# Optimization experiments

Hardware: AMD Instinct MI355X
Metric: run time of the kernel (lower is better)

The kernel has to match this reference:

```python
import jax, jax.numpy as jnp
import numpy as np

HEAD_DIM = 64
NUM_Q_HEADS = 16
NUM_KV_HEADS = 4
MIN_TS = 1.0
MAX_TS = 10000.0


def _timescale(d):
    frac = 2.0 * jnp.arange(d // 2, dtype=jnp.float32) / d
    return MIN_TS * (MAX_TS / MIN_TS) ** frac  # [d/2]


def _rope(v, pos):
    # v: [B,S,H,D] float, pos: [B,S] int
    ts = _timescale(v.shape[-1])
    sinu = pos[:, :, None, None].astype(jnp.float32) / ts  # [B,S,1,D/2]
    sin, cos = jnp.sin(sinu), jnp.cos(sinu)
    x1, x2 = jnp.split(v.astype(jnp.float32), 2, axis=-1)
    return jnp.concatenate([x1 * cos - x2 * sin, x2 * cos + x1 * sin], axis=-1)


def setup_inputs() -> dict:
    key = jax.random.key(0)
    ks = jax.random.split(key, 5)
    B, S, E = 2, 2048, 1024
    Hq, Hk, D = NUM_Q_HEADS, NUM_KV_HEADS, HEAD_DIM
    sc = 0.02
    x = jax.random.normal(ks[0], (B, S, E), dtype=jnp.float32)
    q_pos = jnp.broadcast_to(jnp.arange(S, dtype=jnp.int32), (B, S))
    Wq = jax.random.normal(ks[1], (E, Hq * D), dtype=jnp.float32) * sc
    Wk = jax.random.normal(ks[2], (E, Hk * D), dtype=jnp.float32) * sc
    Wv = jax.random.normal(ks[3], (E, Hk * D), dtype=jnp.float32) * sc
    Wo = jax.random.normal(ks[4], (Hq * D, E), dtype=jnp.float32) * sc
    return {"x": x, "q_pos": q_pos, "Wq": Wq, "Wk": Wk, "Wv": Wv, "Wo": Wo}


def reference(x, q_pos, Wq, Wk, Wv, Wo):
    B, S, E = x.shape
    Hq, Hk, D = NUM_Q_HEADS, NUM_KV_HEADS, HEAD_DIM
    G = Hq // Hk  # gqa groups

    q = (x @ Wq).reshape(B, S, Hq, D)
    k = (x @ Wk).reshape(B, S, Hk, D)
    v = (x @ Wv).reshape(B, S, Hk, D)

    q = _rope(q, q_pos)  # kv_pos defaults to q_pos
    k = _rope(k, q_pos)

    # [B,Hk,G,S,D] grouped query heads vs shared kv heads
    qg = q.transpose(0, 2, 1, 3).reshape(B, Hk, G, S, D)
    kt = k.transpose(0, 2, 1, 3)  # [B,Hk,S,D]
    vt = v.transpose(0, 2, 1, 3)

    # NOTE: original uses scale=1.0 (no 1/sqrt(D))
    scores = jnp.einsum('bhgqd,bhkd->bhgqk', qg, kt)
    probs = jax.nn.softmax(scores, axis=-1)
    out = jnp.einsum('bhgqk,bhkd->bhgqd', probs, vt)  # [B,Hk,G,S,D]
    out = out.reshape(B, Hq, S, D).transpose(0, 2, 1, 3).reshape(B, S, Hq * D)
    return out @ Wo
```

## Files before the change

### kernel.cpp

```cpp
#include <hip/hip_runtime.h>
#include <hip/hip_fp16.h>
#include <math.h>

typedef __attribute__((ext_vector_type(8))) _Float16 half8;
typedef __attribute__((ext_vector_type(4))) _Float16 half4;
typedef __attribute__((ext_vector_type(4))) float f32x4;
typedef __attribute__((ext_vector_type(16))) float f32x16;
typedef __attribute__((ext_vector_type(4))) unsigned uint4v;

#define HQ 16
#define HK 4
#define DH 64
#define NB 2
#define SEQ 2048
#define EDIM 1024
#define KD 1024

__global__ __launch_bounds__(256) void cvt_x_kernel(const float* __restrict__ x,
                                                    _Float16* __restrict__ xh, int n4) {
  int i = blockIdx.x * 256 + threadIdx.x;
  if (i >= n4) return;
  float4 v = ((const float4*)x)[i];
  half4 h;
  h[0] = (_Float16)v.x; h[1] = (_Float16)v.y; h[2] = (_Float16)v.z; h[3] = (_Float16)v.w;
  *(half4*)(xh + (size_t)i * 4) = h;
}

__global__ __launch_bounds__(256) void rope_tab_kernel(const int* __restrict__ qpos,
                                                       float2* __restrict__ tab) {
  int i = blockIdx.x * 256 + threadIdx.x;
  int row = i >> 5, d = i & 31;
  float ang = (float)qpos[row] * expf((float)d * -0.2878231366242558f);
  float sn, cs;
  sincosf(ang, &sn, &cs);
  tab[i] = make_float2(sn, cs);
}

__global__ __launch_bounds__(256) void transpose_w_kernel(const float* __restrict__ W,
                                                          _Float16* __restrict__ WT,
                                                          int N, int row_off) {
  __shared__ float t[64][65];
  int n0 = blockIdx.x * 64, k0 = blockIdx.y * 64;
  int tid = threadIdx.x;
#pragma unroll
  for (int p = 0; p < 4; ++p) {
    int idx = tid + p * 256;
    int r = idx >> 4;
    int c4 = idx & 15;
    float4 v = *(const float4*)(W + (size_t)(k0 + r) * N + n0 + c4 * 4);
    t[r][c4 * 4 + 0] = v.x; t[r][c4 * 4 + 1] = v.y;
    t[r][c4 * 4 + 2] = v.z; t[r][c4 * 4 + 3] = v.w;
  }
  __syncthreads();
#pragma unroll
  for (int p = 0; p < 4; ++p) {
    int idx = tid + p * 256;
    int n = idx >> 4;
    int k4 = idx & 15;
    half4 h;
    h[0] = (_Float16)t[k4 * 4 + 0][n]; h[1] = (_Float16)t[k4 * 4 + 1][n];
    h[2] = (_Float16)t[k4 * 4 + 2][n]; h[3] = (_Float16)t[k4 * 4 + 3][n];
    *(half4*)(WT + (size_t)(row_off + n0 + n) * KD + k0 + k4 * 4) = h;
  }
}

__global__ __launch_bounds__(256) void transpose_v_kernel(const _Float16* __restrict__ vhp,
                                                          _Float16* __restrict__ vtp) {
  __shared__ _Float16 t[64][72];
  int bh = blockIdx.y;
  int s0 = blockIdx.x * 64;
  const _Float16* src = vhp + ((size_t)bh * SEQ + s0) * DH;
  _Float16* dst = vtp + (size_t)bh * DH * SEQ + s0;
  int tid = threadIdx.x;
#pragma unroll
  for (int p = 0; p < 2; ++p) {
    int idx = tid + p * 256;
    int r = idx >> 3, c8 = idx & 7;
    half8 v = *(const half8*)(src + (size_t)r * DH + c8 * 8);
#pragma unroll
    for (int i = 0; i < 8; ++i) t[r][c8 * 8 + i] = v[i];
  }
  __syncthreads();
#pragma unroll
  for (int p = 0; p < 2; ++p) {
    int idx = tid + p * 256;
    int d = idx >> 3, c8 = idx & 7;
    half8 v;
#pragma unroll
    for (int i = 0; i < 8; ++i) v[i] = t[c8 * 8 + i][d];
    *(half8*)(dst + (size_t)d * SEQ + c8 * 8) = v;
  }
}

#define SWZ(r, kb) ((kb) ^ (((r) & 7) << 4))

__global__ __launch_bounds__(256) void gemm_qkv_rope(
    const _Float16* __restrict__ xh, const _Float16* __restrict__ WT,
    const float2* __restrict__ rtab,
    _Float16* __restrict__ qh, _Float16* __restrict__ kh, _Float16* __restrict__ vh) {
  __shared__ char As[128 * 64 * 2];
  __shared__ char Bs[128 * 64 * 2];
  int tid = threadIdx.x, lane = tid & 63, wid = tid >> 6;
  int wr = wid >> 1, wc = wid & 1;
  int bm = blockIdx.x, bn = blockIdx.y;

  const _Float16* Ag = xh + (size_t)bm * 128 * KD;
  const _Float16* Bg = WT + (size_t)bn * 128 * KD;

  f32x4 acc[4][4] = {};

  for (int kt = 0; kt < KD / 64; ++kt) {
#pragma unroll
    for (int p = 0; p < 4; ++p) {
      int idx = tid + p * 256;
      int r = idx >> 3, k8 = idx & 7;
      half8 va = *(const half8*)(Ag + (size_t)r * KD + kt * 64 + k8 * 8);
      *(half8*)(As + r * 128 + SWZ(r, k8 * 16)) = va;
      half8 vb = *(const half8*)(Bg + (size_t)r * KD + kt * 64 + k8 * 8);
      *(half8*)(Bs + r * 128 + SWZ(r, k8 * 16)) = vb;
    }
    __syncthreads();
#pragma unroll
    for (int kk = 0; kk < 2; ++kk) {
      int kb = kk * 64 + (lane >> 4) * 16;
      half8 af[4], bf[4];
#pragma unroll
      for (int mf = 0; mf < 4; ++mf) {
        int r = wr * 64 + mf * 16 + (lane & 15);
        af[mf] = *(const half8*)(As + r * 128 + SWZ(r, kb));
      }
#pragma unroll
      for (int nf = 0; nf < 4; ++nf) {
        int r = wc * 64 + nf * 16 + (lane & 15);
        bf[nf] = *(const half8*)(Bs + r * 128 + SWZ(r, kb));
      }
#pragma unroll
      for (int mf = 0; mf < 4; ++mf)
#pragma unroll
        for (int nf = 0; nf < 4; ++nf)
          acc[mf][nf] = __builtin_amdgcn_mfma_f32_16x16x32_f16(af[mf], bf[nf], acc[mf][nf], 0, 0, 0);
    }
    __syncthreads();
  }

  int col0 = bn * 128 + wc * 64;
  int row_base = bm * 128 + wr * 64;
#pragma unroll
  for (int mf = 0; mf < 4; ++mf) {
#pragma unroll
    for (int j = 0; j < 4; ++j) {
      int row = row_base + mf * 16 + (lane >> 4) * 4 + j;
      int b = row >> 11, s = row & (SEQ - 1);
      if (col0 < 1024) {
        int hq = col0 >> 6;
        size_t base = (((size_t)b * HQ + hq) * SEQ + s) * DH;
#pragma unroll
        for (int nf = 0; nf < 2; ++nf) {
          int d = nf * 16 + (lane & 15);
          float2 scv = rtab[row * 32 + d];
          float x1 = acc[mf][nf][j], x2 = acc[mf][nf + 2][j];
          qh[base + d]      = (_Float16)(x1 * scv.y - x2 * scv.x);
          qh[base + d + 32] = (_Float16)(x2 * scv.y + x1 * scv.x);
        }
      } else if (col0 < 1280) {
        int hk = (col0 - 1024) >> 6;
        size_t base = (((size_t)b * HK + hk) * SEQ + s) * DH;
#pragma unroll
        for (int nf = 0; nf < 2; ++nf) {
          int d = nf * 16 + (lane & 15);
          float2 scv = rtab[row * 32 + d];
          float x1 = acc[mf][nf][j], x2 = acc[mf][nf + 2][j];
          kh[base + d]      = (_Float16)(x1 * scv.y - x2 * scv.x);
          kh[base + d + 32] = (_Float16)(x2 * scv.y + x1 * scv.x);
        }
      } else {
        int hk = (col0 - 1280) >> 6;
        size_t base = (((size_t)b * HK + hk) * SEQ + s) * DH;
#pragma unroll
        for (int nf = 0; nf < 4; ++nf) {
          int d = nf * 16 + (lane & 15);
          vh[base + d] = (_Float16)acc[mf][nf][j];
        }
      }
    }
  }
}

__global__ __launch_bounds__(256) void attn_kernel(
    const _Float16* __restrict__ qh, const _Float16* __restrict__ kh,
    const _Float16* __restrict__ vt, _Float16* __restrict__ oh) {
  __shared__ char Ks[128 * 64 * 2];
  __shared__ char Vs[64 * 128 * 2];

  int tid = threadIdx.x, lane = tid & 63, wid = tid >> 6;
  int half = lane >> 5, l31 = lane & 31;
  bool lopart = (half == 0);
  int qt = blockIdx.x, bh = blockIdx.y;
  int b = bh >> 4, hq = bh & 15, hk = hq >> 2;

  const _Float16* Qg = qh + (((size_t)b * HQ + hq) * SEQ + qt * 128 + wid * 32 + l31) * DH;
  const _Float16* Kg = kh + (((size_t)b * HK + hk) * SEQ) * DH;
  const _Float16* Vtg = vt + (size_t)(b * HK + hk) * DH * SEQ;

  int kr = tid >> 3, kd8 = tid & 7;
  int vr = tid >> 4, vc8 = tid & 15;

  const _Float16 l2e = (_Float16)1.44269504f;
  half8 qf[4];
#pragma unroll
  for (int ks = 0; ks < 4; ++ks) {
    half8 q0 = *(const half8*)(Qg + ks * 16 + half * 8);
#pragma unroll
    for (int i = 0; i < 8; ++i) q0[i] = q0[i] * l2e;
    qf[ks] = q0;
  }

  f32x16 oacc[2] = {};
  float m = -3e38f, l = 0.f;

  for (int kt = 0; kt < SEQ / 128; ++kt) {
#pragma unroll
    for (int p = 0; p < 4; ++p) {
      int r = kr + p * 32;
      *(half8*)(Ks + r * 128 + SWZ(r, kd8 * 16)) =
          *(const half8*)(Kg + (size_t)(kt * 128 + r) * DH + kd8 * 8);
      int d = vr + p * 16;
      *(half8*)(Vs + d * 256 + SWZ(d, vc8 * 16)) =
          *(const half8*)(Vtg + (size_t)d * SEQ + kt * 128 + vc8 * 8);
    }
    __syncthreads();

    f32x16 sacc[4] = {};
    __builtin_amdgcn_s_setprio(1);
#pragma unroll
    for (int b4 = 0; b4 < 4; ++b4) {
      int r = b4 * 32 + l31;
#pragma unroll
      for (int ks = 0; ks < 4; ++ks) {
        half8 kf = *(const half8*)(Ks + r * 128 + SWZ(r, ks * 32 + half * 16));
        sacc[b4] = __builtin_amdgcn_mfma_f32_32x32x16_f16(kf, qf[ks], sacc[b4], 0, 0, 0);
      }
    }
    __builtin_amdgcn_s_setprio(0);

    float pm = sacc[0][0];
#pragma unroll
    for (int b4 = 0; b4 < 4; ++b4)
#pragma unroll
      for (int r = 0; r < 16; ++r)
        if (b4 || r) pm = fmaxf(pm, sacc[b4][r]);
    pm = fmaxf(pm, __shfl_xor(pm, 32, 64));
    float mnew = fmaxf(m, pm);
    float alpha = __builtin_amdgcn_exp2f(m - mnew);
    m = mnew;
    oacc[0] *= alpha;
    oacc[1] *= alpha;
    l *= alpha;
    float ps = 0.f;

#pragma unroll
    for (int b4 = 0; b4 < 4; ++b4) {
      float e[16];
#pragma unroll
      for (int r = 0; r < 16; ++r) {
        e[r] = __builtin_amdgcn_exp2f(sacc[b4][r] - m);
        ps += e[r];
      }
      unsigned W0[4], W1[4];
#pragma unroll
      for (int qd = 0; qd < 4; ++qd) {
        W0[qd] = __builtin_bit_cast(unsigned, __builtin_amdgcn_cvt_pkrtz(e[4 * qd + 0], e[4 * qd + 1]));
        W1[qd] = __builtin_bit_cast(unsigned, __builtin_amdgcn_cvt_pkrtz(e[4 * qd + 2], e[4 * qd + 3]));
      }
      half8 pf[2];
#pragma unroll
      for (int s = 0; s < 2; ++s) {
        unsigned selA = lopart ? W0[2 * s + 1] : W0[2 * s];
        unsigned crA = (unsigned)__shfl_xor((int)selA, 32, 64);
        unsigned selB = lopart ? W1[2 * s + 1] : W1[2 * s];
        unsigned crB = (unsigned)__shfl_xor((int)selB, 32, 64);
        uint4v u;
        u[0] = lopart ? W0[2 * s] : crA;
        u[1] = lopart ? W1[2 * s] : crB;
        u[2] = lopart ? crA : W0[2 * s + 1];
        u[3] = lopart ? crB : W1[2 * s + 1];
        pf[s] = __builtin_bit_cast(half8, u);
      }
      __builtin_amdgcn_s_setprio(1);
#pragma unroll
      for (int s = 0; s < 2; ++s) {
        int kvb = b4 * 64 + s * 32 + half * 16;
#pragma unroll
        for (int dblk = 0; dblk < 2; ++dblk) {
          int d = dblk * 32 + l31;
          half8 vf = *(const half8*)(Vs + d * 256 + SWZ(d, kvb));
          oacc[dblk] = __builtin_amdgcn_mfma_f32_32x32x16_f16(vf, pf[s], oacc[dblk], 0, 0, 0);
        }
      }
      __builtin_amdgcn_s_setprio(0);
    }
    ps += __shfl_xor(ps, 32, 64);
    l += ps;
    __syncthreads();
  }

  int s = qt * 128 + wid * 32 + l31;
  float invl = 1.f / l;
  size_t base = ((size_t)b * SEQ + s) * 1024 + hq * 64;
#pragma unroll
  for (int dblk = 0; dblk < 2; ++dblk) {
#pragma unroll
    for (int qd = 0; qd < 4; ++qd) {
      half4 o;
#pragma unroll
      for (int j = 0; j < 4; ++j) o[j] = (_Float16)(oacc[dblk][qd * 4 + j] * invl);
      *(half4*)(oh + base + dblk * 32 + qd * 8 + half * 4) = o;
    }
  }
}

__global__ __launch_bounds__(256) void gemm_out(
    const _Float16* __restrict__ ah, const _Float16* __restrict__ WoT,
    float* __restrict__ out) {
  __shared__ char As[128 * 64 * 2];
  __shared__ char Bs[128 * 64 * 2];
  int tid = threadIdx.x, lane = tid & 63, wid = tid >> 6;
  int wr = wid >> 1, wc = wid & 1;
  int bm = blockIdx.x, bn = blockIdx.y;
  const _Float16* Ag = ah + (size_t)bm * 128 * KD;
  const _Float16* Bg = WoT + (size_t)bn * 128 * KD;
  f32x4 acc[4][4] = {};

  for (int kt = 0; kt < KD / 64; ++kt) {
#pragma unroll
    for (int p = 0; p < 4; ++p) {
      int idx = tid + p * 256;
      int r = idx >> 3, k8 = idx & 7;
      half8 va = *(const half8*)(Ag + (size_t)r * KD + kt * 64 + k8 * 8);
      *(half8*)(As + r * 128 + SWZ(r, k8 * 16)) = va;
      half8 vb = *(const half8*)(Bg + (size_t)r * KD + kt * 64 + k8 * 8);
      *(half8*)(Bs + r * 128 + SWZ(r, k8 * 16)) = vb;
    }
    __syncthreads();
#pragma unroll
    for (int kk = 0; kk < 2; ++kk) {
      int kb = kk * 64 + (lane >> 4) * 16;
      half8 af[4], bf[4];
#pragma unroll
      for (int mf = 0; mf < 4; ++mf) {
        int r = wr * 64 + mf * 16 + (lane & 15);
        af[mf] = *(const half8*)(As + r * 128 + SWZ(r, kb));
      }
#pragma unroll
      for (int nf = 0; nf < 4; ++nf) {
        int r = wc * 64 + nf * 16 + (lane & 15);
        bf[nf] = *(const half8*)(Bs + r * 128 + SWZ(r, kb));
      }
#pragma unroll
      for (int mf = 0; mf < 4; ++mf)
#pragma unroll
        for (int nf = 0; nf < 4; ++nf)
          acc[mf][nf] = __builtin_amdgcn_mfma_f32_16x16x32_f16(af[mf], bf[nf], acc[mf][nf], 0, 0, 0);
    }
    __syncthreads();
  }

  int row0 = bm * 128 + wr * 64, col0 = bn * 128 + wc * 64;
#pragma unroll
  for (int mf = 0; mf < 4; ++mf)
#pragma unroll
    for (int j = 0; j < 4; ++j) {
      int row = row0 + mf * 16 + (lane >> 4) * 4 + j;
#pragma unroll
      for (int nf = 0; nf < 4; ++nf)
        out[(size_t)row * 1024 + col0 + nf * 16 + (lane & 15)] = acc[mf][nf][j];
    }
}

extern "C" void kernel_launch(void* const* d_in, const int* in_sizes, int n_in,
                              void* d_out, int out_size, void* d_ws, size_t ws_size,
                              hipStream_t stream) {
  const float* x  = (const float*)d_in[0];
  const int* qpos = (const int*)d_in[1];
  const float* Wq = (const float*)d_in[2];
  const float* Wk = (const float*)d_in[3];
  const float* Wv = (const float*)d_in[4];
  const float* Wo = (const float*)d_in[5];
  float* out = (float*)d_out;

  char* ws = (char*)d_ws;
  _Float16* xh  = (_Float16*)(ws);
  _Float16* WT  = (_Float16*)(ws + 8388608);
  _Float16* WoT = (_Float16*)(ws + 11534336);
  _Float16* qhp = (_Float16*)(ws + 13631488);
  _Float16* khp = (_Float16*)(ws + 22020096);
  _Float16* vhp = (_Float16*)(ws + 24117248);
  _Float16* ohp = (_Float16*)(ws + 26214400);
  float2*   rtab = (float2*)(ws + 34603008);
  _Float16* vtp = (_Float16*)(ws + 35651584);

  cvt_x_kernel<<<4096, 256, 0, stream>>>(x, xh, 1048576);
  rope_tab_kernel<<<512, 256, 0, stream>>>(qpos, rtab);
  transpose_w_kernel<<<dim3(16, 16), 256, 0, stream>>>(Wq, WT, 1024, 0);
  transpose_w_kernel<<<dim3(4, 16), 256, 0, stream>>>(Wk, WT, 256, 1024);
  transpose_w_kernel<<<dim3(4, 16), 256, 0, stream>>>(Wv, WT, 256, 1280);
  transpose_w_kernel<<<dim3(16, 16), 256, 0, stream>>>(Wo, WoT, 1024, 0);
  gemm_qkv_rope<<<dim3(32, 12), 256, 0, stream>>>(xh, WT, rtab, qhp, khp, vhp);
  transpose_v_kernel<<<dim3(32, 8), 256, 0, stream>>>(vhp, vtp);
  attn_kernel<<<dim3(16, 32), 256, 0, stream>>>(qhp, khp, vtp, ohp);
  gemm_out<<<dim3(32, 8), 256, 0, stream>>>(ohp, WoT, out);
}
```

Before: 131.3 us.

## Use direct global-to-LDS loads and double-buffer K/V tiles in attention

Replaces the register-staged global→LDS copies in both GEMMs and the attention kernel with 16-byte global_load_lds instructions, pre-swizzling the global addresses so the LDS layout matches the old XOR swizzle. In attention, K/V tiles are now double-buffered: the next tile is prefetched while the current one is computed, with manual vmcnt waits and raw barriers. This aims to cut VGPR staging and hide memory latency behind MFMA work, at the cost of doubled LDS for attention and correctness depending on the hand-written waitcnt/barrier ordering.

```diff
diff --git a/kernel.cpp b/kernel.cpp
--- a/kernel.cpp
+++ b/kernel.cpp
@@ -15,6 +15,12 @@
 #define SEQ 2048
 #define EDIM 1024
 #define KD 1024
+
+__device__ __forceinline__ void gload16(const void* g, void* l) {
+  __builtin_amdgcn_global_load_lds(
+      (const __attribute__((address_space(1))) void*)g,
+      (__attribute__((address_space(3))) void*)l, 16, 0, 0);
+}
 
 __global__ __launch_bounds__(256) void cvt_x_kernel(const float* __restrict__ x,
                                                     _Float16* __restrict__ xh, int n4) {
@@ -104,20 +110,20 @@
   int wr = wid >> 1, wc = wid & 1;
   int bm = blockIdx.x, bn = blockIdx.y;
 
-  const _Float16* Ag = xh + (size_t)bm * 128 * KD;
-  const _Float16* Bg = WT + (size_t)bn * 128 * KD;
+  const char* Ag = (const char*)(xh + (size_t)bm * 128 * KD);
+  const char* Bg = (const char*)(WT + (size_t)bn * 128 * KD);
+
+  int colS = 16 * ((lane & 7) ^ (lane >> 3));
+  int rS = (lane >> 3);
 
   f32x4 acc[4][4] = {};
 
   for (int kt = 0; kt < KD / 64; ++kt) {
 #pragma unroll
     for (int p = 0; p < 4; ++p) {
-      int idx = tid + p * 256;
-      int r = idx >> 3, k8 = idx & 7;
-      half8 va = *(const half8*)(Ag + (size_t)r * KD + kt * 64 + k8 * 8);
-      *(half8*)(As + r * 128 + SWZ(r, k8 * 16)) = va;
-      half8 vb = *(const half8*)(Bg + (size_t)r * KD + kt * 64 + k8 * 8);
-      *(half8*)(Bs + r * 128 + SWZ(r, k8 * 16)) = vb;
+      int r = (wid * 4 + p) * 8 + rS;
+      gload16(Ag + (size_t)r * (KD * 2) + kt * 128 + colS, As + (wid * 4 + p) * 1024);
+      gload16(Bg + (size_t)r * (KD * 2) + kt * 128 + colS, Bs + (wid * 4 + p) * 1024);
     }
     __syncthreads();
 #pragma unroll
@@ -189,8 +195,8 @@
 __global__ __launch_bounds__(256) void attn_kernel(
     const _Float16* __restrict__ qh, const _Float16* __restrict__ kh,
     const _Float16* __restrict__ vt, _Float16* __restrict__ oh) {
-  __shared__ char Ks[128 * 64 * 2];
-  __shared__ char Vs[64 * 128 * 2];
+  __shared__ char Ks[2][128 * 64 * 2];
+  __shared__ char Vs[2][64 * 128 * 2];
 
   int tid = threadIdx.x, lane = tid & 63, wid = tid >> 6;
   int half = lane >> 5, l31 = lane & 31;
@@ -199,11 +205,8 @@
   int b = bh >> 4, hq = bh & 15, hk = hq >> 2;
 
   const _Float16* Qg = qh + (((size_t)b * HQ + hq) * SEQ + qt * 128 + wid * 32 + l31) * DH;
-  const _Float16* Kg = kh + (((size_t)b * HK + hk) * SEQ) * DH;
-  const _Float16* Vtg = vt + (size_t)(b * HK + hk) * DH * SEQ;
-
-  int kr = tid >> 3, kd8 = tid & 7;
-  int vr = tid >> 4, vc8 = tid & 15;
+  const char* Kg = (const char*)(kh + (((size_t)b * HK + hk) * SEQ) * DH);
+  const char* Vtg = (const char*)(vt + (size_t)(b * HK + hk) * DH * SEQ);
 
   const _Float16 l2e = (_Float16)1.44269504f;
   half8 qf[4];
@@ -215,20 +218,41 @@
     qf[ks] = q0;
   }
 
+  int colK = 16 * ((lane & 7) ^ (lane >> 3));
+  int rK = lane >> 3;
+
   f32x16 oacc[2] = {};
   float m = -3e38f, l = 0.f;
 
+#pragma unroll
+  for (int p = 0; p < 4; ++p) {
+    int r = (wid * 4 + p) * 8 + rK;
+    gload16(Kg + (size_t)r * 128 + colK, Ks[0] + (wid * 4 + p) * 1024);
+    int d = (wid * 4 + p) * 4 + (lane >> 4);
+    int colV = ((lane & 15) * 16) ^ ((d & 7) << 4);
+    gload16(Vtg + (size_t)d * (SEQ * 2) + colV, Vs[0] + (wid * 4 + p) * 1024);
+  }
+
+  int cur = 0;
   for (int kt = 0; kt < SEQ / 128; ++kt) {
-#pragma unroll
-    for (int p = 0; p < 4; ++p) {
-      int r = kr + p * 32;
-      *(half8*)(Ks + r * 128 + SWZ(r, kd8 * 16)) =
-          *(const half8*)(Kg + (size_t)(kt * 128 + r) * DH + kd8 * 8);
-      int d = vr + p * 16;
-      *(half8*)(Vs + d * 256 + SWZ(d, vc8 * 16)) =
-          *(const half8*)(Vtg + (size_t)d * SEQ + kt * 128 + vc8 * 8);
-    }
-    __syncthreads();
+    if (kt + 1 < SEQ / 128) {
+#pragma unroll
+      for (int p = 0; p < 4; ++p) {
+        int r = (wid * 4 + p) * 8 + rK;
+        gload16(Kg + (size_t)((kt + 1) * 128 + r) * 128 + colK,
+                Ks[cur ^ 1] + (wid * 4 + p) * 1024);
+        int d = (wid * 4 + p) * 4 + (lane >> 4);
+        int colV = ((lane & 15) * 16) ^ ((d & 7) << 4);
+        gload16(Vtg + (size_t)d * (SEQ * 2) + (kt + 1) * 256 + colV,
+                Vs[cur ^ 1] + (wid * 4 + p) * 1024);
+      }
+      asm volatile("s_waitcnt vmcnt(8)" ::: "memory");
+    } else {
+      asm volatile("s_waitcnt vmcnt(0)" ::: "memory");
+    }
+    __builtin_amdgcn_s_barrier();
+    const char* KsB = Ks[cur];
+    const char* VsB = Vs[cur];
 
     f32x16 sacc[4] = {};
     __builtin_amdgcn_s_setprio(1);
@@ -237,7 +261,7 @@
       int r = b4 * 32 + l31;
 #pragma unroll
       for (int ks = 0; ks < 4; ++ks) {
-        half8 kf = *(const half8*)(Ks + r * 128 + SWZ(r, ks * 32 + half * 16));
+        half8 kf = *(const half8*)(KsB + r * 128 + SWZ(r, ks * 32 + half * 16));
         sacc[b4] = __builtin_amdgcn_mfma_f32_32x32x16_f16(kf, qf[ks], sacc[b4], 0, 0, 0);
       }
     }
@@ -293,7 +317,7 @@
 #pragma unroll
         for (int dblk = 0; dblk < 2; ++dblk) {
           int d = dblk * 32 + l31;
-          half8 vf = *(const half8*)(Vs + d * 256 + SWZ(d, kvb));
+          half8 vf = *(const half8*)(VsB + d * 256 + SWZ(d, kvb));
           oacc[dblk] = __builtin_amdgcn_mfma_f32_32x32x16_f16(vf, pf[s], oacc[dblk], 0, 0, 0);
         }
       }
@@ -301,7 +325,8 @@
     }
     ps += __shfl_xor(ps, 32, 64);
     l += ps;
-    __syncthreads();
+    __builtin_amdgcn_s_barrier();
+    cur ^= 1;
   }
 
   int s = qt * 128 + wid * 32 + l31;
@@ -327,19 +352,18 @@
   int tid = threadIdx.x, lane = tid & 63, wid = tid >> 6;
   int wr = wid >> 1, wc = wid & 1;
   int bm = blockIdx.x, bn = blockIdx.y;
-  const _Float16* Ag = ah + (size_t)bm * 128 * KD;
-  const _Float16* Bg = WoT + (size_t)bn * 128 * KD;
+  const char* Ag = (const char*)(ah + (size_t)bm * 128 * KD);
+  const char* Bg = (const char*)(WoT + (size_t)bn * 128 * KD);
+  int colS = 16 * ((lane & 7) ^ (lane >> 3));
+  int rS = (lane >> 3);
   f32x4 acc[4][4] = {};
 
   for (int kt = 0; kt < KD / 64; ++kt) {
 #pragma unroll
     for (int p = 0; p < 4; ++p) {
-      int idx = tid + p * 256;
-      int r = idx >> 3, k8 = idx & 7;
-      half8 va = *(const half8*)(Ag + (size_t)r * KD + kt * 64 + k8 * 8);
-      *(half8*)(As + r * 128 + SWZ(r, k8 * 16)) = va;
-      half8 vb = *(const half8*)(Bg + (size_t)r * KD + kt * 64 + k8 * 8);
-      *(half8*)(Bs + r * 128 + SWZ(r, k8 * 16)) = vb;
+      int r = (wid * 4 + p) * 8 + rS;
+      gload16(Ag + (size_t)r * (KD * 2) + kt * 128 + colS, As + (wid * 4 + p) * 1024);
+      gload16(Bg + (size_t)r * (KD * 2) + kt * 128 + colS, Bs + (wid * 4 + p) * 1024);
     }
     __syncthreads();
 #pragma unroll
```

Result: faster. 128.7 us (-2.0%).
